# Kernel tuning notes

Hardware: AMD Instinct MI355X
Metric: run time of the kernel (lower is better)

The kernel has to match this reference:

```python
import jax, jax.numpy as jnp
import numpy as np

T, B, L, CTX, H = 512, 512, 16, 64, 128
STATE_DIM, SHOT, PID, DATA = 32, 12, 35, 23


def setup_inputs() -> dict:
    key = jax.random.key(0)
    ks = jax.random.split(key, 64)
    k = iter(ks)
    def rn(shape, s=0.1):
        return (jax.random.normal(next(k), shape) * s).astype(jnp.float32)
    xs = jax.random.normal(next(k), (T, B, DATA), jnp.float32)
    xs = xs.at[:, :, 12].set(jax.random.randint(next(k), (T, B), 0, SHOT).astype(jnp.float32))
    xs = xs.at[:, :, 17].set(jax.random.randint(next(k), (T, B), 0, PID).astype(jnp.float32))
    xs = xs.at[:, :, 20].set(jax.random.randint(next(k), (T, B), 0, SHOT).astype(jnp.float32))
    return dict(
        total_xs=jnp.zeros((1,), jnp.float32),
        xs=xs,
        ts=jnp.linspace(0.0, 2.0, T).astype(jnp.float32),
        noise_std=jnp.asarray(0.1, jnp.float32),
        z0_noise=jax.random.normal(next(k), (B, L), jnp.float32),
        bm_noise=jax.random.normal(next(k), (T - 1, B, L), jnp.float32),
        shot_emb=rn((SHOT, 8)), player_emb=rn((PID, 8)),
        gru_wih=rn((3 * H, STATE_DIM)), gru_whh=rn((3 * H, H)),
        gru_bih=rn((3 * H,)), gru_bhh=rn((3 * H,)),
        enc_w=rn((CTX, H)), enc_b=rn((CTX,)),
        qz0_w=rn((2 * L, CTX)), qz0_b=rn((2 * L,)),
        f_w1=rn((H, L + CTX)), f_b1=rn((H,)), f_w2=rn((H, H)), f_b2=rn((H,)),
        f_w3=rn((L, H)), f_b3=rn((L,)),
        h_w1=rn((H, L)), h_b1=rn((H,)), h_w2=rn((H, H)), h_b2=rn((H,)),
        h_w3=rn((L, H)), h_b3=rn((L,)),
        g_w1=rn((L, H)), g_b1=rn((L, H)), g_w2=rn((L, H)), g_b2=rn((L,)),
        proj_w=rn((STATE_DIM, L)), proj_b=rn((STATE_DIM,)),
        pz0_mean=jnp.zeros((1, L), jnp.float32), pz0_logstd=jnp.zeros((1, L), jnp.float32),
        act_w=rn((128, L)), act_b=rn((128,)),
        act_land_w=rn((2, 128)), act_shot_w=rn((SHOT, 128)), act_move_w=rn((2, 128)),
    )


def _forward(xs, noise_std, shot_emb, player_emb, gru_wih, gru_whh, gru_bih, gru_bhh,
             enc_w, enc_b, qz0_w, qz0_b,
             f_w1, f_b1, f_w2, f_b2, f_w3, f_b3,
             h_w1, h_b1, h_w2, h_b2, h_w3, h_b3,
             g_w1, g_b1, g_w2, g_b2,
             proj_w, proj_b, pz0_mean, pz0_logstd,
             act_w, act_b, act_land_w, act_shot_w, act_move_w,
             ts, z0_noise, bm_noise):
    # --- SDE_embed_and_transform: replace shot/player id cols with embeddings ---
    state = xs[:, :, :18]
    shot_ids = state[:, :, 12].astype(jnp.int32)
    pid_ids = state[:, :, 17].astype(jnp.int32)
    state_t = jnp.concatenate([state[:, :, :12], shot_emb[shot_ids],
                               state[:, :, 13:17], player_emb[pid_ids]], axis=-1)  # (T,B,32)
    xs_t = jnp.concatenate([state_t, xs[:, :, 18:]], axis=-1)  # (T,B,37)
    # --- Encoder: GRU over time-reversed states, linear head, flip back ---
    def gru_step(h, xt):
        gi = xt @ gru_wih.T + gru_bih
        gh = h @ gru_whh.T + gru_bhh
        ir, iz, inn = jnp.split(gi, 3, axis=-1)
        hr, hz, hn = jnp.split(gh, 3, axis=-1)
        r = jax.nn.sigmoid(ir + hr)
        zg = jax.nn.sigmoid(iz + hz)
        n = jnp.tanh(inn + r * hn)
        hnew = (1.0 - zg) * n + zg * h
        return hnew, hnew
    h0 = jnp.zeros((xs.shape[1], gru_whh.shape[1]), xs.dtype)
    _, hs = jax.lax.scan(gru_step, h0, state_t[::-1])
    ctx = (hs @ enc_w.T + enc_b)[::-1]  # (T,B,CTX)
    # --- posterior z0 ---
    qm, qls = jnp.split(ctx[0] @ qz0_w.T + qz0_b, 2, axis=1)
    z0 = qm + jnp.exp(qls) * z0_noise
    # --- Euler-Maruyama with logqp; searchsorted(right) -> ctx[min(i+1,T-1)] = ctx[i+1] ---
    dts = ts[1:] - ts[:-1]  # (T-1,)
    dW = jnp.sqrt(dts)[:, None, None] * bm_noise
    ctx_steps = ctx[1:]
    def mlp3(x, w1, b1, w2, b2, w3, b3):
        h1 = jax.nn.softplus(x @ w1.T + b1)
        h2 = jax.nn.softplus(h1 @ w2.T + b2)
        return h2 @ w3.T + b3
    def g_diag(y):  # (B,L): per-latent-dim scalar nets, batched over L
        hg = jax.nn.softplus(y[:, :, None] * g_w1[None] + g_b1[None])  # (B,L,H)
        return jax.nn.sigmoid(jnp.einsum('blh,lh->bl', hg, g_w2) + g_b2)
    def sde_step(z, inp):
        c, dw, dt = inp
        f_val = mlp3(jnp.concatenate([z, c], axis=1), f_w1, f_b1, f_w2, f_b2, f_w3, f_b3)
        h_val = mlp3(z, h_w1, h_b1, h_w2, h_b2, h_w3, h_b3)
        g_val = g_diag(z)
        u = (f_val - h_val) / g_val
        logr = 0.5 * jnp.sum(u * u, axis=1) * dt
        z_new = z + f_val * dt + g_val * dw
        return z_new, (z_new, logr)
    _, (z_tail, log_ratio) = jax.lax.scan(sde_step, z0, (ctx_steps, dW, dts))
    zs = jnp.concatenate([z0[None], z_tail], axis=0)  # (T,B,L)
    _xs = zs @ proj_w.T + proj_b  # (T,B,32)
    # --- action model losses ---
    a = jax.nn.relu(zs @ act_w.T + act_b)
    land = (a @ act_land_w.T).reshape(-1, 2)
    shot_logits = (a @ act_shot_w.T).reshape(-1, act_shot_w.shape[0])
    move = (a @ act_move_w.T).reshape(-1, 2)
    true_actions = xs_t[:, :, -5:]
    true_land = true_actions[:, :, :2].reshape(-1, 2)
    true_move = true_actions[:, :, 3:].reshape(-1, 2)
    true_shot = true_actions[:, :, 2].astype(jnp.int32).reshape(-1)
    land_loss = jnp.mean((land - true_land) ** 2)
    move_loss = jnp.mean((move - true_move) ** 2)
    logp = jax.nn.log_softmax(shot_logits, axis=-1)
    picked = jnp.take_along_axis(logp, true_shot[:, None], axis=1)[:, 0]
    mask = (true_shot != 0).astype(logp.dtype)  # CrossEntropy ignore_index=0
    shot_loss = -jnp.sum(picked * mask) / jnp.maximum(jnp.sum(mask), 1.0)
    # --- reconstruction log-likelihood ---
    xs_state = xs_t[:, :, :STATE_DIM]
    LOG2PI = 1.8378770664093453
    log_pxs = jnp.mean(jnp.sum(
        -0.5 * ((xs_state - _xs) / noise_std) ** 2 - jnp.log(noise_std) - 0.5 * LOG2PI,
        axis=(0, 2)))
    # --- KL(q(z0) || p(z0)) ---
    var_q = jnp.exp(2.0 * qls)
    var_p = jnp.exp(2.0 * pz0_logstd)
    kl = pz0_logstd - qls + (var_q + (qm - pz0_mean) ** 2) / (2.0 * var_p) - 0.5
    logqp0 = jnp.mean(jnp.sum(kl, axis=1))
    logqp_path = jnp.mean(jnp.sum(log_ratio, axis=0))
    return log_pxs, logqp0 + logqp_path + land_loss + shot_loss + move_loss


def reference(total_xs, xs, ts, noise_std, z0_noise, bm_noise, shot_emb, player_emb,
              gru_wih, gru_whh, gru_bih, gru_bhh, enc_w, enc_b, qz0_w, qz0_b,
              f_w1, f_b1, f_w2, f_b2, f_w3, f_b3, h_w1, h_b1, h_w2, h_b2, h_w3, h_b3,
              g_w1, g_b1, g_w2, g_b2, proj_w, proj_b, pz0_mean, pz0_logstd,
              act_w, act_b, act_land_w, act_shot_w, act_move_w):
    return _forward(xs, noise_std, shot_emb, player_emb, gru_wih, gru_whh, gru_bih, gru_bhh,
                    enc_w, enc_b, qz0_w, qz0_b,
                    f_w1, f_b1, f_w2, f_b2, f_w3, f_b3,
                    h_w1, h_b1, h_w2, h_b2, h_w3, h_b3,
                    g_w1, g_b1, g_w2, g_b2,
                    proj_w, proj_b, pz0_mean, pz0_logstd,
                    act_w, act_b, act_land_w, act_shot_w, act_move_w,
                    ts, z0_noise, bm_noise)
```

## Files before the change

kernel.cpp:

```cpp
#include <hip/hip_runtime.h>
#include <cstdint>

typedef _Float16 f16;
typedef _Float16 f16x2 __attribute__((ext_vector_type(2)));

#define T_STEPS 512
#define B_SZ 512
#define LOG2PI 1.8378770664093453f

__device__ __forceinline__ uint32_t packh2(float a, float b) {
  f16x2 v; v[0] = (f16)a; v[1] = (f16)b;
  return __builtin_bit_cast(uint32_t, v);
}

__device__ __forceinline__ float fdot2(uint32_t a, uint32_t b, float c) {
#if defined(__AMDGCN__) && __has_builtin(__builtin_amdgcn_fdot2)
  return __builtin_amdgcn_fdot2(__builtin_bit_cast(f16x2, a),
                                __builtin_bit_cast(f16x2, b), c, false);
#else
  f16x2 x = __builtin_bit_cast(f16x2, a), y = __builtin_bit_cast(f16x2, b);
  return c + (float)x[0] * (float)y[0] + (float)x[1] * (float)y[1];
#endif
}

#define DOT4(acc, w0, w1, w2, w3, v)                                     \
  do {                                                                   \
    acc = fdot2((w0), (v).x, acc); acc = fdot2((w1), (v).y, acc);        \
    acc = fdot2((w2), (v).z, acc); acc = fdot2((w3), (v).w, acc);        \
  } while (0)

__device__ __forceinline__ float sigmoidf_(float x) {
  return 1.0f / (1.0f + __expf(-x));
}
__device__ __forceinline__ float tanhf_(float x) {
  float ax = fabsf(x);
  float t = __expf(-2.0f * ax);
  float r = (1.0f - t) / (1.0f + t);
  return copysignf(r, x);
}
__device__ __forceinline__ float softplusf_(float x) {
  return fmaxf(x, 0.0f) + __logf(1.0f + __expf(-fabsf(x)));
}

__global__ __launch_bounds__(256) void k_embed(
    const float* __restrict__ xs, const float* __restrict__ shot_emb,
    const float* __restrict__ player_emb, f16* __restrict__ state_t,
    float* __restrict__ accums) {
  if (blockIdx.x == 0 && threadIdx.x < 16) accums[threadIdx.x] = 0.0f;
  size_t idx = (size_t)blockIdx.x * 256 + threadIdx.x;
  const float* xp = xs + idx * 23;
  f16* op = state_t + idx * 32;
  int sid = (int)xp[12];
  int pid = (int)xp[17];
#pragma unroll
  for (int i = 0; i < 12; ++i) op[i] = (f16)xp[i];
  const float* se = shot_emb + sid * 8;
#pragma unroll
  for (int i = 0; i < 8; ++i) op[12 + i] = (f16)se[i];
#pragma unroll
  for (int i = 0; i < 4; ++i) op[20 + i] = (f16)xp[13 + i];
  const float* pe = player_emb + pid * 8;
#pragma unroll
  for (int i = 0; i < 8; ++i) op[24 + i] = (f16)pe[i];
}

__global__ __launch_bounds__(512) void k_gru(
    const f16* __restrict__ state_t, const float* __restrict__ wih,
    const float* __restrict__ whh, const float* __restrict__ bih,
    const float* __restrict__ bhh, const float* __restrict__ enc_w,
    const float* __restrict__ enc_b, const float* __restrict__ qz0_w,
    const float* __restrict__ qz0_b, const float* __restrict__ z0_noise,
    const float* __restrict__ pz0_mean, const float* __restrict__ pz0_logstd,
    f16* __restrict__ ctx, float* __restrict__ z0_out,
    float* __restrict__ accums) {
  __shared__ uint32_t s_x[2][16];
  __shared__ uint32_t s_h[2][64];
  __shared__ float s_gates[2 * 128 * 4];
  __shared__ float s_encp[2 * 64 * 2];
  __shared__ float s_ctx0[2][64];
  __shared__ float s_q[2][32];

  const int tid = threadIdx.x;
  const int bbase = blockIdx.x * 2;
  const uint32_t* stu = (const uint32_t*)state_t;

  uint32_t wA[64];
  uint32_t wB[16];
  float bias0 = 0.f, bias1 = 0.f, encbr = 0.f;

  if (tid < 256) {
    int g = tid >> 7, du = tid & 127;
    const float* whr = whh + (size_t)(g * 128 + du) * 128;
#pragma unroll
    for (int i = 0; i < 64; ++i) wA[i] = packh2(whr[2 * i], whr[2 * i + 1]);
    const float* wxr = wih + (size_t)(g * 128 + du) * 32;
#pragma unroll
    for (int i = 0; i < 16; ++i) wB[i] = packh2(wxr[2 * i], wxr[2 * i + 1]);
    bias0 = bih[g * 128 + du] + bhh[g * 128 + du];
  } else if (tid < 384) {
    int du = tid - 256;
    const float* whr = whh + (size_t)(256 + du) * 128;
#pragma unroll
    for (int i = 0; i < 64; ++i) wA[i] = packh2(whr[2 * i], whr[2 * i + 1]);
    const float* wxr = wih + (size_t)(256 + du) * 32;
#pragma unroll
    for (int i = 0; i < 16; ++i) wB[i] = packh2(wxr[2 * i], wxr[2 * i + 1]);
    bias0 = bih[256 + du];
    bias1 = bhh[256 + du];
  } else {
    int e = tid - 384, c = e & 63, ks = e >> 6;
    const float* wer = enc_w + (size_t)c * 128 + ks * 64;
#pragma unroll
    for (int i = 0; i < 32; ++i) wA[i] = packh2(wer[2 * i], wer[2 * i + 1]);
    encbr = enc_b[c];
  }

  if (tid < 128) s_h[tid >> 6][tid & 63] = 0u;
  if (tid < 32) {
    int b = tid >> 4, i = tid & 15;
    s_x[b][i] = stu[((size_t)(T_STEPS - 1) * B_SZ + bbase + b) * 16 + i];
  }
  float h_old = 0.0f;
  __syncthreads();

  for (int t = T_STEPS - 1; t >= 0; --t) {
    uint4 xpref = make_uint4(0, 0, 0, 0);
    if (tid < 256) {
      int g = tid >> 7, du = tid & 127;
#pragma unroll
      for (int b = 0; b < 2; ++b) {
        float a = bias0;
        const uint4* xq = (const uint4*)&s_x[b][0];
#pragma unroll
        for (int j = 0; j < 4; ++j) {
          uint4 v = xq[j];
          DOT4(a, wB[4 * j], wB[4 * j + 1], wB[4 * j + 2], wB[4 * j + 3], v);
        }
        const uint4* hq = (const uint4*)&s_h[b][0];
#pragma unroll
        for (int j = 0; j < 16; ++j) {
          uint4 v = hq[j];
          DOT4(a, wA[4 * j], wA[4 * j + 1], wA[4 * j + 2], wA[4 * j + 3], v);
        }
        s_gates[(b * 128 + du) * 4 + g] = a;
      }
    } else if (tid < 384) {
      int du = tid - 256;
#pragma unroll
      for (int b = 0; b < 2; ++b) {
        float aI = bias0, aH = bias1;
        const uint4* xq = (const uint4*)&s_x[b][0];
#pragma unroll
        for (int j = 0; j < 4; ++j) {
          uint4 v = xq[j];
          DOT4(aI, wB[4 * j], wB[4 * j + 1], wB[4 * j + 2], wB[4 * j + 3], v);
        }
        const uint4* hq = (const uint4*)&s_h[b][0];
#pragma unroll
        for (int j = 0; j < 16; ++j) {
          uint4 v = hq[j];
          DOT4(aH, wA[4 * j], wA[4 * j + 1], wA[4 * j + 2], wA[4 * j + 3], v);
        }
        s_gates[(b * 128 + du) * 4 + 2] = aI;
        s_gates[(b * 128 + du) * 4 + 3] = aH;
      }
    } else {
      int e = tid - 384, ks = e >> 6, cc = e & 63;
      (void)cc;
      if (t < T_STEPS - 1) {
#pragma unroll
        for (int b = 0; b < 2; ++b) {
          float a = 0.f;
          const uint4* hq = (const uint4*)&s_h[b][ks * 32];
#pragma unroll
          for (int j = 0; j < 8; ++j) {
            uint4 v = hq[j];
            DOT4(a, wA[4 * j], wA[4 * j + 1], wA[4 * j + 2], wA[4 * j + 3], v);
          }
          s_encp[(b * 64 + cc) * 2 + ks] = a;
        }
      }
      if (e < 8 && t > 0) {
        int b = e & 1, q = e >> 1;
        xpref = *(const uint4*)(stu +
                                ((size_t)(t - 1) * B_SZ + bbase + b) * 16 + q * 4);
      }
    }
    __syncthreads();
    if (tid < 256) {
      int b = tid >> 7, du = tid & 127;
      const float4 gt = *(const float4*)&s_gates[(b * 128 + du) * 4];
      float r = sigmoidf_(gt.x), zg = sigmoidf_(gt.y);
      float n = tanhf_(gt.z + r * gt.w);
      float hnew = (1.0f - zg) * n + zg * h_old;
      h_old = hnew;
      ((f16*)&s_h[b][0])[du] = (f16)hnew;
    } else if (tid >= 384) {
      int e = tid - 384, cc = e & 63, b = e >> 6;
      if (t < T_STEPS - 1) {
        float2 p = *(const float2*)&s_encp[(b * 64 + cc) * 2];
        ctx[((size_t)(t + 1) * B_SZ + bbase + b) * 64 + cc] =
            (f16)(p.x + p.y + encbr);
      }
      if (e < 8 && t > 0) {
        int b2 = e & 1, q = e >> 1;
        *(uint4*)&s_x[b2][q * 4] = xpref;
      }
    }
    __syncthreads();
  }

  if (tid >= 384) {
    int e = tid - 384, ks = e >> 6, cc = e & 63;
#pragma unroll
    for (int b = 0; b < 2; ++b) {
      float a = 0.f;
      const uint4* hq = (const uint4*)&s_h[b][ks * 32];
#pragma unroll
      for (int j = 0; j < 8; ++j) {
        uint4 v = hq[j];
        DOT4(a, wA[4 * j], wA[4 * j + 1], wA[4 * j + 2], wA[4 * j + 3], v);
      }
      s_encp[(b * 64 + cc) * 2 + ks] = a;
    }
  }
  __syncthreads();
  if (tid >= 384) {
    int e = tid - 384, cc = e & 63, b = e >> 6;
    float2 p = *(const float2*)&s_encp[(b * 64 + cc) * 2];
    float val = p.x + p.y + encbr;
    ctx[((size_t)bbase + b) * 64 + cc] = (f16)val;
    s_ctx0[b][cc] = val;
  }
  __syncthreads();
  if (tid < 64) {
    int b = tid >> 5, o = tid & 31;
    float acc = qz0_b[o];
#pragma unroll 8
    for (int k = 0; k < 64; ++k) acc += qz0_w[o * 64 + k] * s_ctx0[b][k];
    s_q[b][o] = acc;
  }
  __syncthreads();
  if (tid < 32) {
    int b = tid >> 4, l = tid & 15;
    int bg = bbase + b;
    float qm = s_q[b][l], qls = s_q[b][16 + l];
    float z0v = qm + __expf(qls) * z0_noise[bg * 16 + l];
    z0_out[bg * 16 + l] = z0v;
    float pm = pz0_mean[l], pls = pz0_logstd[l];
    float var_q = __expf(2.0f * qls);
    float var_p = __expf(2.0f * pls);
    float dm = qm - pm;
    float kl = pls - qls + (var_q + dm * dm) / (2.0f * var_p) - 0.5f;
    atomicAdd(&accums[5], kl);
  }
}

__global__ __launch_bounds__(512) void k_sde(
    const f16* __restrict__ ctx, const float* __restrict__ z0_in,
    const float* __restrict__ ts, const float* __restrict__ bm_noise,
    const float* __restrict__ fw1, const float* __restrict__ fb1,
    const float* __restrict__ fw2, const float* __restrict__ fb2,
    const float* __restrict__ fw3, const float* __restrict__ fb3,
    const float* __restrict__ hw1, const float* __restrict__ hb1,
    const float* __restrict__ hw2, const float* __restrict__ hb2,
    const float* __restrict__ hw3, const float* __restrict__ hb3,
    const float* __restrict__ gw1, const float* __restrict__ gb1,
    const float* __restrict__ gw2, const float* __restrict__ gb2,
    f16* __restrict__ zs, float* __restrict__ accums) {
  __shared__ uint32_t s_x2[2][40];
  __shared__ float s_zf[2][16];
  __shared__ uint32_t s_h1[2][2][64];
  __shared__ uint32_t s_h2[2][2][64];
  __shared__ float s_gp[256];
  __shared__ float s_gv[32];
  __shared__ float s_p2[2 * 2 * 128 * 2];
  __shared__ float s_p3[2 * 2 * 16 * 8];
  __shared__ float s_dts[512];

  const int tid = threadIdx.x;
  const int bbase = blockIdx.x * 2;

  uint32_t uw[48];
  uint32_t wP2[32];
  uint32_t wP3[8];
  float bias1r = 0.f, bias2r = 0.f, gb2r = 0.f, fb3r = 0.f, hb3r = 0.f;

  if (tid < 256) {
    int l = tid & 15, k8 = (tid >> 4) & 7;
#pragma unroll
    for (int i = 0; i < 16; ++i) {
      int h = k8 * 16 + i;
      uw[i] = __builtin_bit_cast(uint32_t, gw1[l * 128 + h]);
      uw[16 + i] = __builtin_bit_cast(uint32_t, gb1[l * 128 + h]);
      uw[32 + i] = __builtin_bit_cast(uint32_t, gw2[l * 128 + h]);
    }
  } else if (tid < 384) {
    int u = tid - 256;
    const float* w = fw1 + (size_t)u * 80;
#pragma unroll
    for (int i = 0; i < 40; ++i) uw[i] = packh2(w[2 * i], w[2 * i + 1]);
    bias1r = fb1[u];
  } else {
    int u = tid - 384;
    const float* w = hw1 + (size_t)u * 16;
#pragma unroll
    for (int i = 0; i < 8; ++i) uw[i] = packh2(w[2 * i], w[2 * i + 1]);
    bias1r = hb1[u];
  }
  {
    int u = tid & 127, ks = (tid >> 7) & 1, mlp = tid >> 8;
    const float* w = (mlp ? hw2 : fw2) + (size_t)u * 128 + ks * 64;
#pragma unroll
    for (int i = 0; i < 32; ++i) wP2[i] = packh2(w[2 * i], w[2 * i + 1]);
    bias2r = (mlp ? hb2 : fb2)[u];
  }
  if (tid < 128 || (tid >= 256 && tid < 384)) {
    int o = tid & 15, k8 = (tid >> 4) & 7;
    const float* w = ((tid >= 256) ? hw3 : fw3) + (size_t)o * 128 + k8 * 16;
#pragma unroll
    for (int i = 0; i < 8; ++i) wP3[i] = packh2(w[2 * i], w[2 * i + 1]);
  }
  if (tid >= 128 && tid < 160) gb2r = gb2[tid & 15];
  if (tid < 32) {
    fb3r = fb3[tid & 15];
    hb3r = hb3[tid & 15];
  }

  if (tid < 511) s_dts[tid] = ts[tid + 1] - ts[tid];
  float bmc = 0.f;
  uint4 cpref = make_uint4(0, 0, 0, 0);
  if (tid < 32) {
    int b = tid >> 4, l = tid & 15, bg = bbase + b;
    float z = z0_in[bg * 16 + l];
    s_zf[b][l] = z;
    ((f16*)&s_x2[b][0])[l] = (f16)z;
    zs[(size_t)bg * 16 + l] = (f16)z;
    bmc = bm_noise[((size_t)0 * B_SZ + bg) * 16 + l];
  }
  if (tid >= 32 && tid < 48) {
    int i = tid - 32, b = i & 1, q = i >> 1;
    const uint32_t* cu = (const uint32_t*)ctx;
    uint4 v = *(const uint4*)(cu + ((size_t)1 * B_SZ + bbase + b) * 32 + q * 4);
    *(uint4*)&s_x2[b][8 + q * 4] = v;
  }
  float path_acc = 0.0f;
  __syncthreads();

  for (int t = 0; t < T_STEPS - 1; ++t) {
    float bmn = 0.f;
    if (tid < 32 && t < T_STEPS - 2) {
      int b = tid >> 4, l = tid & 15, bg = bbase + b;
      bmn = bm_noise[((size_t)(t + 1) * B_SZ + bg) * 16 + l];
    }
    if (tid >= 32 && tid < 48 && t <= T_STEPS - 3) {
      int i = tid - 32, b = i & 1, q = i >> 1;
      const uint32_t* cu = (const uint32_t*)ctx;
      cpref = *(const uint4*)(cu +
                              ((size_t)(t + 2) * B_SZ + bbase + b) * 32 + q * 4);
    }
    if (tid < 256) {
      int b = tid >> 7, l = tid & 15, k8 = (tid >> 4) & 7;
      float y = s_zf[b][l];
      float acc = 0.f;
#pragma unroll
      for (int i = 0; i < 16; ++i) {
        float pre = fmaf(y, __builtin_bit_cast(float, uw[i]),
                         __builtin_bit_cast(float, uw[16 + i]));
        acc = fmaf(softplusf_(pre), __builtin_bit_cast(float, uw[32 + i]), acc);
      }
      s_gp[(b * 16 + l) * 8 + k8] = acc;
    } else if (tid < 384) {
      int u = tid - 256;
#pragma unroll
      for (int b = 0; b < 2; ++b) {
        float a = bias1r;
        const uint4* xq = (const uint4*)&s_x2[b][0];
#pragma unroll
        for (int j = 0; j < 10; ++j) {
          uint4 v = xq[j];
          DOT4(a, uw[4 * j], uw[4 * j + 1], uw[4 * j + 2], uw[4 * j + 3], v);
        }
        ((f16*)&s_h1[0][b][0])[u] = (f16)softplusf_(a);
      }
    } else {
      int u = tid - 384;
#pragma unroll
      for (int b = 0; b < 2; ++b) {
        float a = bias1r;
        const uint4* xq = (const uint4*)&s_x2[b][0];
#pragma unroll
        for (int j = 0; j < 2; ++j) {
          uint4 v = xq[j];
          DOT4(a, uw[4 * j], uw[4 * j + 1], uw[4 * j + 2], uw[4 * j + 3], v);
        }
        ((f16*)&s_h1[1][b][0])[u] = (f16)softplusf_(a);
      }
    }
    __syncthreads();
    {
      int u = tid & 127, ks = (tid >> 7) & 1, mlp = tid >> 8;
#pragma unroll
      for (int b = 0; b < 2; ++b) {
        float a = 0.f;
        const uint4* hq = (const uint4*)&s_h1[mlp][b][ks * 32];
#pragma unroll
        for (int j = 0; j < 8; ++j) {
          uint4 v = hq[j];
          DOT4(a, wP2[4 * j], wP2[4 * j + 1], wP2[4 * j + 2], wP2[4 * j + 3], v);
        }
        s_p2[((mlp * 2 + b) * 128 + u) * 2 + ks] = a;
      }
    }
    __syncthreads();
    {
      int u = tid & 127, b = (tid >> 7) & 1, mlp = tid >> 8;
      float2 p = *(const float2*)&s_p2[((mlp * 2 + b) * 128 + u) * 2];
      ((f16*)&s_h2[mlp][b][0])[u] = (f16)softplusf_(p.x + p.y + bias2r);
    }
    __syncthreads();
    if (tid < 128 || (tid >= 256 && tid < 384)) {
      int o = tid & 15, k8 = (tid >> 4) & 7, mlp = tid >> 8;
#pragma unroll
      for (int b = 0; b < 2; ++b) {
        float a = 0.f;
        const uint4* hq = (const uint4*)&s_h2[mlp][b][k8 * 8];
#pragma unroll
        for (int j = 0; j < 2; ++j) {
          uint4 v = hq[j];
          DOT4(a, wP3[4 * j], wP3[4 * j + 1], wP3[4 * j + 2], wP3[4 * j + 3], v);
        }
        s_p3[((mlp * 2 + b) * 16 + o) * 8 + k8] = a;
      }
    } else if (tid >= 128 && tid < 160) {
      int i = tid - 128, b = i >> 4, l = i & 15;
      const float4* gp = (const float4*)&s_gp[(b * 16 + l) * 8];
      float4 g0 = gp[0], g1 = gp[1];
      float sum = g0.x + g0.y + g0.z + g0.w + g1.x + g1.y + g1.z + g1.w + gb2r;
      s_gv[b * 16 + l] = sigmoidf_(sum);
    }
    __syncthreads();
    if (tid < 32) {
      int b = tid >> 4, l = tid & 15, bg = bbase + b;
      const float4* fp = (const float4*)&s_p3[((0 * 2 + b) * 16 + l) * 8];
      const float4* hp = (const float4*)&s_p3[((2 + b) * 16 + l) * 8];
      float4 f0 = fp[0], f1v = fp[1], h0 = hp[0], h1v = hp[1];
      float fv = fb3r + f0.x + f0.y + f0.z + f0.w + f1v.x + f1v.y + f1v.z + f1v.w;
      float hv = hb3r + h0.x + h0.y + h0.z + h0.w + h1v.x + h1v.y + h1v.z + h1v.w;
      float gv = s_gv[b * 16 + l];
      float dt = s_dts[t];
      float u = (fv - hv) / gv;
      float lsum = u * u;
      lsum += __shfl_xor(lsum, 1);
      lsum += __shfl_xor(lsum, 2);
      lsum += __shfl_xor(lsum, 4);
      lsum += __shfl_xor(lsum, 8);
      if (l == 0) path_acc += 0.5f * lsum * dt;
      float dw = sqrtf(dt) * bmc;
      float zn = s_zf[b][l] + fv * dt + gv * dw;
      s_zf[b][l] = zn;
      ((f16*)&s_x2[b][0])[l] = (f16)zn;
      zs[((size_t)(t + 1) * B_SZ + bg) * 16 + l] = (f16)zn;
      bmc = bmn;
    } else if (tid >= 32 && tid < 48 && t <= T_STEPS - 3) {
      int i = tid - 32, b = i & 1, q = i >> 1;
      *(uint4*)&s_x2[b][8 + q * 4] = cpref;
    }
    __syncthreads();
  }
  if (tid < 32 && (tid & 15) == 0) atomicAdd(&accums[6], path_acc);
}

__global__ __launch_bounds__(256) void k_dec(
    const f16* __restrict__ zs, const f16* __restrict__ state_t,
    const float* __restrict__ xs, const float* __restrict__ proj_w,
    const float* __restrict__ proj_b, const float* __restrict__ act_w,
    const float* __restrict__ act_b, const float* __restrict__ land_w,
    const float* __restrict__ shot_w, const float* __restrict__ move_w,
    float* __restrict__ accums) {
  __shared__ uint32_t s_proj[8 * 32];
  __shared__ uint32_t s_act[8 * 128];
  __shared__ uint32_t s_head[128 * 8];
  __shared__ float s_pb[32], s_ab[128];
  __shared__ float s_red[4 * 5];

  const int tid = threadIdx.x;
  for (int id = tid; id < 8 * 32; id += 256) {
    int kp = id & 7, n = id >> 3;
    s_proj[kp * 32 + n] = packh2(proj_w[n * 16 + 2 * kp], proj_w[n * 16 + 2 * kp + 1]);
  }
  for (int id = tid; id < 8 * 128; id += 256) {
    int kp = id & 7, n = id >> 3;
    s_act[kp * 128 + n] = packh2(act_w[n * 16 + 2 * kp], act_w[n * 16 + 2 * kp + 1]);
  }
  for (int id = tid; id < 128 * 8; id += 256) {
    int j = id >> 3, p = id & 7;
    int h0 = 2 * p, h1 = 2 * p + 1;
    float w0 = (h0 < 2) ? land_w[h0 * 128 + j]
                        : (h0 < 14 ? shot_w[(h0 - 2) * 128 + j]
                                   : move_w[(h0 - 14) * 128 + j]);
    float w1 = (h1 < 2) ? land_w[h1 * 128 + j]
                        : (h1 < 14 ? shot_w[(h1 - 2) * 128 + j]
                                   : move_w[(h1 - 14) * 128 + j]);
    s_head[j * 8 + p] = packh2(w0, w1);
  }
  if (tid < 32) s_pb[tid] = proj_b[tid];
  if (tid < 128) s_ab[tid] = act_b[tid];
  __syncthreads();

  size_t idx = (size_t)blockIdx.x * 256 + tid;
  uint32_t z2[8];
  const uint32_t* zp = (const uint32_t*)(zs + idx * 16);
#pragma unroll
  for (int i = 0; i < 8; ++i) z2[i] = zp[i];
  uint32_t stv[16];
  const uint32_t* stp = (const uint32_t*)(state_t + idx * 32);
#pragma unroll
  for (int i = 0; i < 16; ++i) stv[i] = stp[i];

  float sqsum = 0.0f;
#pragma unroll 4
  for (int i = 0; i < 32; ++i) {
    float acc = s_pb[i];
#pragma unroll
    for (int kp = 0; kp < 8; ++kp) acc = fdot2(s_proj[kp * 32 + i], z2[kp], acc);
    f16x2 sv = __builtin_bit_cast(f16x2, stv[i >> 1]);
    float d = (float)sv[i & 1] - acc;
    sqsum += d * d;
  }

  float hd[16];
#pragma unroll
  for (int i = 0; i < 16; ++i) hd[i] = 0.0f;
#pragma unroll 2
  for (int j = 0; j < 128; ++j) {
    float a = s_ab[j];
#pragma unroll
    for (int kp = 0; kp < 8; ++kp) a = fdot2(s_act[kp * 128 + j], z2[kp], a);
    a = fmaxf(a, 0.0f);
#pragma unroll
    for (int p = 0; p < 8; ++p) {
      f16x2 w = __builtin_bit_cast(f16x2, s_head[j * 8 + p]);
      hd[2 * p] += (float)w[0] * a;
      hd[2 * p + 1] += (float)w[1] * a;
    }
  }
  const float* xp = xs + idx * 23;
  float dl0 = hd[0] - xp[18], dl1 = hd[1] - xp[19];
  float land = dl0 * dl0 + dl1 * dl1;
  float dm0 = hd[14] - xp[21], dm1 = hd[15] - xp[22];
  float move = dm0 * dm0 + dm1 * dm1;
  int sid = (int)xp[20];
  float m = hd[2];
#pragma unroll
  for (int s = 1; s < 12; ++s) m = fmaxf(m, hd[2 + s]);
  float sume = 0.0f;
#pragma unroll
  for (int s = 0; s < 12; ++s) sume += __expf(hd[2 + s] - m);
  float lse = m + __logf(sume);
  float pl = 0.0f;
#pragma unroll
  for (int s = 0; s < 12; ++s)
    if (s == sid) pl = hd[2 + s];
  float picked = 0.0f, cnt = 0.0f;
  if (sid != 0) {
    picked = pl - lse;
    cnt = 1.0f;
  }
  float vals[5] = {sqsum, land, move, picked, cnt};
#pragma unroll
  for (int v = 0; v < 5; ++v) {
    float x = vals[v];
    for (int off = 1; off < 64; off <<= 1) x += __shfl_xor(x, off);
    vals[v] = x;
  }
  int lane = tid & 63, wv = tid >> 6;
  if (lane == 0) {
#pragma unroll
    for (int v = 0; v < 5; ++v) s_red[wv * 5 + v] = vals[v];
  }
  __syncthreads();
  if (tid == 0) {
#pragma unroll
    for (int v = 0; v < 5; ++v) {
      float s = s_red[v] + s_red[5 + v] + s_red[10 + v] + s_red[15 + v];
      atomicAdd(&accums[v], s);
    }
  }
}

__global__ void k_fin(const float* __restrict__ accums,
                      const float* __restrict__ noise_std,
                      float* __restrict__ out) {
  if (threadIdx.x == 0 && blockIdx.x == 0) {
    float sd = noise_std[0];
    float log_pxs = -0.5f * accums[0] / (sd * sd * (float)B_SZ) -
                    (float)T_STEPS * 32.0f * (logf(sd) + 0.5f * LOG2PI);
    float land = accums[1] / (float)(T_STEPS * B_SZ * 2);
    float move = accums[2] / (float)(T_STEPS * B_SZ * 2);
    float shot = -accums[3] / fmaxf(accums[4], 1.0f);
    float out1 = accums[5] / (float)B_SZ + accums[6] / (float)B_SZ + land + shot + move;
    out[0] = log_pxs;
    out[1] = out1;
  }
}

extern "C" void kernel_launch(void* const* d_in, const int* in_sizes, int n_in,
                              void* d_out, int out_size, void* d_ws,
                              size_t ws_size, hipStream_t stream) {
  const float* xs = (const float*)d_in[1];
  const float* ts = (const float*)d_in[2];
  const float* noise_std = (const float*)d_in[3];
  const float* z0_noise = (const float*)d_in[4];
  const float* bm_noise = (const float*)d_in[5];
  const float* shot_emb = (const float*)d_in[6];
  const float* player_emb = (const float*)d_in[7];
  const float* gru_wih = (const float*)d_in[8];
  const float* gru_whh = (const float*)d_in[9];
  const float* gru_bih = (const float*)d_in[10];
  const float* gru_bhh = (const float*)d_in[11];
  const float* enc_w = (const float*)d_in[12];
  const float* enc_b = (const float*)d_in[13];
  const float* qz0_w = (const float*)d_in[14];
  const float* qz0_b = (const float*)d_in[15];
  const float* f_w1 = (const float*)d_in[16];
  const float* f_b1 = (const float*)d_in[17];
  const float* f_w2 = (const float*)d_in[18];
  const float* f_b2 = (const float*)d_in[19];
  const float* f_w3 = (const float*)d_in[20];
  const float* f_b3 = (const float*)d_in[21];
  const float* h_w1 = (const float*)d_in[22];
  const float* h_b1 = (const float*)d_in[23];
  const float* h_w2 = (const float*)d_in[24];
  const float* h_b2 = (const float*)d_in[25];
  const float* h_w3 = (const float*)d_in[26];
  const float* h_b3 = (const float*)d_in[27];
  const float* g_w1 = (const float*)d_in[28];
  const float* g_b1 = (const float*)d_in[29];
  const float* g_w2 = (const float*)d_in[30];
  const float* g_b2 = (const float*)d_in[31];
  const float* proj_w = (const float*)d_in[32];
  const float* proj_b = (const float*)d_in[33];
  const float* pz0_mean = (const float*)d_in[34];
  const float* pz0_logstd = (const float*)d_in[35];
  const float* act_w = (const float*)d_in[36];
  const float* act_b = (const float*)d_in[37];
  const float* act_land_w = (const float*)d_in[38];
  const float* act_shot_w = (const float*)d_in[39];
  const float* act_move_w = (const float*)d_in[40];

  char* ws = (char*)d_ws;
  float* accums = (float*)ws;
  f16* state_t = (f16*)(ws + 256);
  f16* ctx = (f16*)(ws + 256 + 16777216);
  float* z0b = (float*)(ws + 256 + 16777216 + 33554432);
  f16* zs = (f16*)(ws + 256 + 16777216 + 33554432 + 32768);

  k_embed<<<1024, 256, 0, stream>>>(xs, shot_emb, player_emb, state_t, accums);
  k_gru<<<256, 512, 0, stream>>>(state_t, gru_wih, gru_whh, gru_bih, gru_bhh,
                                 enc_w, enc_b, qz0_w, qz0_b, z0_noise, pz0_mean,
                                 pz0_logstd, ctx, z0b, accums);
  k_sde<<<256, 512, 0, stream>>>(ctx, z0b, ts, bm_noise, f_w1, f_b1, f_w2, f_b2,
                                 f_w3, f_b3, h_w1, h_b1, h_w2, h_b2, h_w3, h_b3,
                                 g_w1, g_b1, g_w2, g_b2, zs, accums);
  k_dec<<<1024, 256, 0, stream>>>(zs, state_t, xs, proj_w, proj_b, act_w, act_b,
                                  act_land_w, act_shot_w, act_move_w, accums);
  k_fin<<<1, 64, 0, stream>>>(accums, noise_std, (float*)d_out);
}
```

Before: 1.999 ms.

## Assign one batch element per block in GRU and SDE, two tokens per thread in decoder

The GRU and SDE recurrent kernels change from two batch elements per block to one, doubling the grid to 512 blocks and shrinking block sizes (448 and 256 threads) with occupancy launch bounds. Each thread now does a full-length dot product with two split accumulators, which removes the partial-sum scratch buffers and gate interleaving. The decoder processes two tokens per thread with vectorized shared-memory weight layouts, reusing each weight load across both tokens. The aim is more parallelism across CUs and shorter serial dependency chains per recurrence step. The cost is more registers per thread and duplicated weight loading across twice as many blocks.

```diff
diff --git a/kernel.cpp b/kernel.cpp
--- a/kernel.cpp
+++ b/kernel.cpp
@@ -64,7 +64,7 @@
   for (int i = 0; i < 8; ++i) op[24 + i] = (f16)pe[i];
 }
 
-__global__ __launch_bounds__(512) void k_gru(
+__global__ __launch_bounds__(448, 4) void k_gru(
     const f16* __restrict__ state_t, const float* __restrict__ wih,
     const float* __restrict__ whh, const float* __restrict__ bih,
     const float* __restrict__ bhh, const float* __restrict__ enc_w,
@@ -73,181 +73,121 @@
     const float* __restrict__ pz0_mean, const float* __restrict__ pz0_logstd,
     f16* __restrict__ ctx, float* __restrict__ z0_out,
     float* __restrict__ accums) {
-  __shared__ uint32_t s_x[2][16];
-  __shared__ uint32_t s_h[2][64];
-  __shared__ float s_gates[2 * 128 * 4];
-  __shared__ float s_encp[2 * 64 * 2];
-  __shared__ float s_ctx0[2][64];
-  __shared__ float s_q[2][32];
+  __shared__ __align__(16) uint32_t s_x[16];
+  __shared__ __align__(16) uint32_t s_h[64];
+  __shared__ float s_gi[384], s_gh[384];
+  __shared__ float s_ctx0[64];
+  __shared__ float s_q[32];
 
   const int tid = threadIdx.x;
-  const int bbase = blockIdx.x * 2;
+  const int bg = blockIdx.x;
   const uint32_t* stu = (const uint32_t*)state_t;
 
   uint32_t wA[64];
   uint32_t wB[16];
-  float bias0 = 0.f, bias1 = 0.f, encbr = 0.f;
-
-  if (tid < 256) {
-    int g = tid >> 7, du = tid & 127;
-    const float* whr = whh + (size_t)(g * 128 + du) * 128;
+  float bi = 0.f, bh = 0.f, encbr = 0.f;
+
+  if (tid < 384) {
+    const float* whr = whh + (size_t)tid * 128;
 #pragma unroll
     for (int i = 0; i < 64; ++i) wA[i] = packh2(whr[2 * i], whr[2 * i + 1]);
-    const float* wxr = wih + (size_t)(g * 128 + du) * 32;
+    const float* wxr = wih + (size_t)tid * 32;
 #pragma unroll
     for (int i = 0; i < 16; ++i) wB[i] = packh2(wxr[2 * i], wxr[2 * i + 1]);
-    bias0 = bih[g * 128 + du] + bhh[g * 128 + du];
-  } else if (tid < 384) {
-    int du = tid - 256;
-    const float* whr = whh + (size_t)(256 + du) * 128;
-#pragma unroll
-    for (int i = 0; i < 64; ++i) wA[i] = packh2(whr[2 * i], whr[2 * i + 1]);
-    const float* wxr = wih + (size_t)(256 + du) * 32;
-#pragma unroll
-    for (int i = 0; i < 16; ++i) wB[i] = packh2(wxr[2 * i], wxr[2 * i + 1]);
-    bias0 = bih[256 + du];
-    bias1 = bhh[256 + du];
+    bi = bih[tid];
+    bh = bhh[tid];
   } else {
-    int e = tid - 384, c = e & 63, ks = e >> 6;
-    const float* wer = enc_w + (size_t)c * 128 + ks * 64;
-#pragma unroll
-    for (int i = 0; i < 32; ++i) wA[i] = packh2(wer[2 * i], wer[2 * i + 1]);
-    encbr = enc_b[c];
-  }
-
-  if (tid < 128) s_h[tid >> 6][tid & 63] = 0u;
-  if (tid < 32) {
-    int b = tid >> 4, i = tid & 15;
-    s_x[b][i] = stu[((size_t)(T_STEPS - 1) * B_SZ + bbase + b) * 16 + i];
-  }
+    int cc = tid - 384;
+    const float* wer = enc_w + (size_t)cc * 128;
+#pragma unroll
+    for (int i = 0; i < 64; ++i) wA[i] = packh2(wer[2 * i], wer[2 * i + 1]);
+    encbr = enc_b[cc];
+  }
+
+  if (tid < 64) s_h[tid] = 0u;
+  if (tid < 4)
+    *(uint4*)&s_x[tid * 4] =
+        *(const uint4*)(stu + ((size_t)(T_STEPS - 1) * B_SZ + bg) * 16 + tid * 4);
   float h_old = 0.0f;
   __syncthreads();
 
   for (int t = T_STEPS - 1; t >= 0; --t) {
     uint4 xpref = make_uint4(0, 0, 0, 0);
-    if (tid < 256) {
-      int g = tid >> 7, du = tid & 127;
-#pragma unroll
-      for (int b = 0; b < 2; ++b) {
-        float a = bias0;
-        const uint4* xq = (const uint4*)&s_x[b][0];
-#pragma unroll
-        for (int j = 0; j < 4; ++j) {
-          uint4 v = xq[j];
-          DOT4(a, wB[4 * j], wB[4 * j + 1], wB[4 * j + 2], wB[4 * j + 3], v);
-        }
-        const uint4* hq = (const uint4*)&s_h[b][0];
-#pragma unroll
-        for (int j = 0; j < 16; ++j) {
-          uint4 v = hq[j];
-          DOT4(a, wA[4 * j], wA[4 * j + 1], wA[4 * j + 2], wA[4 * j + 3], v);
-        }
-        s_gates[(b * 128 + du) * 4 + g] = a;
+    if (tid >= 128 && tid < 132 && t > 0)
+      xpref = *(const uint4*)(stu + ((size_t)(t - 1) * B_SZ + bg) * 16 +
+                              (tid - 128) * 4);
+    if (tid < 384) {
+      float ax0 = bi, ax1 = 0.f;
+      const uint4* xq = (const uint4*)s_x;
+#pragma unroll
+      for (int j = 0; j < 4; ++j) {
+        uint4 v = xq[j];
+        if (j & 1) { DOT4(ax1, wB[4 * j], wB[4 * j + 1], wB[4 * j + 2], wB[4 * j + 3], v); }
+        else       { DOT4(ax0, wB[4 * j], wB[4 * j + 1], wB[4 * j + 2], wB[4 * j + 3], v); }
       }
-    } else if (tid < 384) {
-      int du = tid - 256;
-#pragma unroll
-      for (int b = 0; b < 2; ++b) {
-        float aI = bias0, aH = bias1;
-        const uint4* xq = (const uint4*)&s_x[b][0];
-#pragma unroll
-        for (int j = 0; j < 4; ++j) {
-          uint4 v = xq[j];
-          DOT4(aI, wB[4 * j], wB[4 * j + 1], wB[4 * j + 2], wB[4 * j + 3], v);
-        }
-        const uint4* hq = (const uint4*)&s_h[b][0];
-#pragma unroll
-        for (int j = 0; j < 16; ++j) {
-          uint4 v = hq[j];
-          DOT4(aH, wA[4 * j], wA[4 * j + 1], wA[4 * j + 2], wA[4 * j + 3], v);
-        }
-        s_gates[(b * 128 + du) * 4 + 2] = aI;
-        s_gates[(b * 128 + du) * 4 + 3] = aH;
+      float ah0 = bh, ah1 = 0.f;
+      const uint4* hq = (const uint4*)s_h;
+#pragma unroll
+      for (int j = 0; j < 16; ++j) {
+        uint4 v = hq[j];
+        if (j & 1) { DOT4(ah1, wA[4 * j], wA[4 * j + 1], wA[4 * j + 2], wA[4 * j + 3], v); }
+        else       { DOT4(ah0, wA[4 * j], wA[4 * j + 1], wA[4 * j + 2], wA[4 * j + 3], v); }
       }
-    } else {
-      int e = tid - 384, ks = e >> 6, cc = e & 63;
-      (void)cc;
-      if (t < T_STEPS - 1) {
-#pragma unroll
-        for (int b = 0; b < 2; ++b) {
-          float a = 0.f;
-          const uint4* hq = (const uint4*)&s_h[b][ks * 32];
-#pragma unroll
-          for (int j = 0; j < 8; ++j) {
-            uint4 v = hq[j];
-            DOT4(a, wA[4 * j], wA[4 * j + 1], wA[4 * j + 2], wA[4 * j + 3], v);
-          }
-          s_encp[(b * 64 + cc) * 2 + ks] = a;
-        }
+      s_gi[tid] = ax0 + ax1;
+      s_gh[tid] = ah0 + ah1;
+    } else if (t < T_STEPS - 1) {
+      int cc = tid - 384;
+      float a0 = encbr, a1 = 0.f;
+      const uint4* hq = (const uint4*)s_h;
+#pragma unroll
+      for (int j = 0; j < 16; ++j) {
+        uint4 v = hq[j];
+        if (j & 1) { DOT4(a1, wA[4 * j], wA[4 * j + 1], wA[4 * j + 2], wA[4 * j + 3], v); }
+        else       { DOT4(a0, wA[4 * j], wA[4 * j + 1], wA[4 * j + 2], wA[4 * j + 3], v); }
       }
-      if (e < 8 && t > 0) {
-        int b = e & 1, q = e >> 1;
-        xpref = *(const uint4*)(stu +
-                                ((size_t)(t - 1) * B_SZ + bbase + b) * 16 + q * 4);
-      }
+      ctx[((size_t)(t + 1) * B_SZ + bg) * 64 + cc] = (f16)(a0 + a1);
     }
     __syncthreads();
-    if (tid < 256) {
-      int b = tid >> 7, du = tid & 127;
-      const float4 gt = *(const float4*)&s_gates[(b * 128 + du) * 4];
-      float r = sigmoidf_(gt.x), zg = sigmoidf_(gt.y);
-      float n = tanhf_(gt.z + r * gt.w);
+    if (tid < 128) {
+      float r = sigmoidf_(s_gi[tid] + s_gh[tid]);
+      float zg = sigmoidf_(s_gi[128 + tid] + s_gh[128 + tid]);
+      float n = tanhf_(s_gi[256 + tid] + r * s_gh[256 + tid]);
       float hnew = (1.0f - zg) * n + zg * h_old;
       h_old = hnew;
-      ((f16*)&s_h[b][0])[du] = (f16)hnew;
-    } else if (tid >= 384) {
-      int e = tid - 384, cc = e & 63, b = e >> 6;
-      if (t < T_STEPS - 1) {
-        float2 p = *(const float2*)&s_encp[(b * 64 + cc) * 2];
-        ctx[((size_t)(t + 1) * B_SZ + bbase + b) * 64 + cc] =
-            (f16)(p.x + p.y + encbr);
-      }
-      if (e < 8 && t > 0) {
-        int b2 = e & 1, q = e >> 1;
-        *(uint4*)&s_x[b2][q * 4] = xpref;
-      }
+      ((f16*)s_h)[tid] = (f16)hnew;
+    } else if (tid >= 128 && tid < 132 && t > 0) {
+      *(uint4*)&s_x[(tid - 128) * 4] = xpref;
     }
     __syncthreads();
   }
 
   if (tid >= 384) {
-    int e = tid - 384, ks = e >> 6, cc = e & 63;
-#pragma unroll
-    for (int b = 0; b < 2; ++b) {
-      float a = 0.f;
-      const uint4* hq = (const uint4*)&s_h[b][ks * 32];
-#pragma unroll
-      for (int j = 0; j < 8; ++j) {
-        uint4 v = hq[j];
-        DOT4(a, wA[4 * j], wA[4 * j + 1], wA[4 * j + 2], wA[4 * j + 3], v);
-      }
-      s_encp[(b * 64 + cc) * 2 + ks] = a;
-    }
-  }
-  __syncthreads();
-  if (tid >= 384) {
-    int e = tid - 384, cc = e & 63, b = e >> 6;
-    float2 p = *(const float2*)&s_encp[(b * 64 + cc) * 2];
-    float val = p.x + p.y + encbr;
-    ctx[((size_t)bbase + b) * 64 + cc] = (f16)val;
-    s_ctx0[b][cc] = val;
-  }
-  __syncthreads();
-  if (tid < 64) {
-    int b = tid >> 5, o = tid & 31;
-    float acc = qz0_b[o];
-#pragma unroll 8
-    for (int k = 0; k < 64; ++k) acc += qz0_w[o * 64 + k] * s_ctx0[b][k];
-    s_q[b][o] = acc;
+    int cc = tid - 384;
+    float a0 = encbr, a1 = 0.f;
+    const uint4* hq = (const uint4*)s_h;
+#pragma unroll
+    for (int j = 0; j < 16; ++j) {
+      uint4 v = hq[j];
+      if (j & 1) { DOT4(a1, wA[4 * j], wA[4 * j + 1], wA[4 * j + 2], wA[4 * j + 3], v); }
+      else       { DOT4(a0, wA[4 * j], wA[4 * j + 1], wA[4 * j + 2], wA[4 * j + 3], v); }
+    }
+    float val = a0 + a1;
+    ctx[(size_t)bg * 64 + cc] = (f16)val;
+    s_ctx0[cc] = val;
   }
   __syncthreads();
   if (tid < 32) {
-    int b = tid >> 4, l = tid & 15;
-    int bg = bbase + b;
-    float qm = s_q[b][l], qls = s_q[b][16 + l];
-    float z0v = qm + __expf(qls) * z0_noise[bg * 16 + l];
-    z0_out[bg * 16 + l] = z0v;
-    float pm = pz0_mean[l], pls = pz0_logstd[l];
+    float acc = qz0_b[tid];
+#pragma unroll 8
+    for (int k = 0; k < 64; ++k) acc += qz0_w[tid * 64 + k] * s_ctx0[k];
+    s_q[tid] = acc;
+  }
+  __syncthreads();
+  if (tid < 16) {
+    float qm = s_q[tid], qls = s_q[16 + tid];
+    float z0v = qm + __expf(qls) * z0_noise[bg * 16 + tid];
+    z0_out[bg * 16 + tid] = z0v;
+    float pm = pz0_mean[tid], pls = pz0_logstd[tid];
     float var_q = __expf(2.0f * qls);
     float var_p = __expf(2.0f * pls);
     float dm = qm - pm;
@@ -256,7 +196,7 @@
   }
 }
 
-__global__ __launch_bounds__(512) void k_sde(
+__global__ __launch_bounds__(256, 2) void k_sde(
     const f16* __restrict__ ctx, const float* __restrict__ z0_in,
     const float* __restrict__ ts, const float* __restrict__ bm_noise,
     const float* __restrict__ fw1, const float* __restrict__ fb1,
@@ -268,186 +208,153 @@
     const float* __restrict__ gw1, const float* __restrict__ gb1,
     const float* __restrict__ gw2, const float* __restrict__ gb2,
     f16* __restrict__ zs, float* __restrict__ accums) {
-  __shared__ uint32_t s_x2[2][40];
-  __shared__ float s_zf[2][16];
-  __shared__ uint32_t s_h1[2][2][64];
-  __shared__ uint32_t s_h2[2][2][64];
-  __shared__ float s_gp[256];
-  __shared__ float s_gv[32];
-  __shared__ float s_p2[2 * 2 * 128 * 2];
-  __shared__ float s_p3[2 * 2 * 16 * 8];
-  __shared__ float s_dts[512];
+  __shared__ __align__(16) uint32_t s_x2[40];
+  __shared__ __align__(16) uint32_t s_h1f[64];
+  __shared__ __align__(16) uint32_t s_h1h[64];
+  __shared__ __align__(16) uint32_t s_h2[2][64];
+  __shared__ float s_zf[16];
+  __shared__ __align__(16) float s_gp[128];
+  __shared__ __align__(16) float s_p3[256];
+  __shared__ float s_dts[T_STEPS];
 
   const int tid = threadIdx.x;
-  const int bbase = blockIdx.x * 2;
-
-  uint32_t uw[48];
-  uint32_t wP2[32];
+  const int bg = blockIdx.x;
+
+  uint32_t uw[56];
+  uint32_t wP2[64];
   uint32_t wP3[8];
   float bias1r = 0.f, bias2r = 0.f, gb2r = 0.f, fb3r = 0.f, hb3r = 0.f;
 
-  if (tid < 256) {
-    int l = tid & 15, k8 = (tid >> 4) & 7;
+  if (tid < 128) {
+    const float* w = fw1 + (size_t)tid * 80;
+#pragma unroll
+    for (int i = 0; i < 40; ++i) uw[i] = packh2(w[2 * i], w[2 * i + 1]);
+    bias1r = fb1[tid];
+  } else {
+    int u = tid - 128;
+    const float* w = hw1 + (size_t)u * 16;
+#pragma unroll
+    for (int i = 0; i < 8; ++i) uw[i] = packh2(w[2 * i], w[2 * i + 1]);
+    bias1r = hb1[u];
+    int l = u & 15, k8 = u >> 4;
 #pragma unroll
     for (int i = 0; i < 16; ++i) {
       int h = k8 * 16 + i;
-      uw[i] = __builtin_bit_cast(uint32_t, gw1[l * 128 + h]);
-      uw[16 + i] = __builtin_bit_cast(uint32_t, gb1[l * 128 + h]);
-      uw[32 + i] = __builtin_bit_cast(uint32_t, gw2[l * 128 + h]);
-    }
-  } else if (tid < 384) {
-    int u = tid - 256;
-    const float* w = fw1 + (size_t)u * 80;
-#pragma unroll
-    for (int i = 0; i < 40; ++i) uw[i] = packh2(w[2 * i], w[2 * i + 1]);
-    bias1r = fb1[u];
-  } else {
-    int u = tid - 384;
-    const float* w = hw1 + (size_t)u * 16;
-#pragma unroll
-    for (int i = 0; i < 8; ++i) uw[i] = packh2(w[2 * i], w[2 * i + 1]);
-    bias1r = hb1[u];
+      uw[8 + i] = __builtin_bit_cast(uint32_t, gw1[l * 128 + h]);
+      uw[24 + i] = __builtin_bit_cast(uint32_t, gb1[l * 128 + h]);
+      uw[40 + i] = __builtin_bit_cast(uint32_t, gw2[l * 128 + h]);
+    }
   }
   {
-    int u = tid & 127, ks = (tid >> 7) & 1, mlp = tid >> 8;
-    const float* w = (mlp ? hw2 : fw2) + (size_t)u * 128 + ks * 64;
-#pragma unroll
-    for (int i = 0; i < 32; ++i) wP2[i] = packh2(w[2 * i], w[2 * i + 1]);
+    int mlp = tid >> 7, u = tid & 127;
+    const float* w = (mlp ? hw2 : fw2) + (size_t)u * 128;
+#pragma unroll
+    for (int i = 0; i < 64; ++i) wP2[i] = packh2(w[2 * i], w[2 * i + 1]);
     bias2r = (mlp ? hb2 : fb2)[u];
   }
-  if (tid < 128 || (tid >= 256 && tid < 384)) {
-    int o = tid & 15, k8 = (tid >> 4) & 7;
-    const float* w = ((tid >= 256) ? hw3 : fw3) + (size_t)o * 128 + k8 * 16;
+  {
+    int mlp = tid >> 7, o = tid & 15, k8 = (tid >> 4) & 7;
+    const float* w = (mlp ? hw3 : fw3) + (size_t)o * 128 + k8 * 16;
 #pragma unroll
     for (int i = 0; i < 8; ++i) wP3[i] = packh2(w[2 * i], w[2 * i + 1]);
   }
-  if (tid >= 128 && tid < 160) gb2r = gb2[tid & 15];
-  if (tid < 32) {
-    fb3r = fb3[tid & 15];
-    hb3r = hb3[tid & 15];
-  }
-
-  if (tid < 511) s_dts[tid] = ts[tid + 1] - ts[tid];
-  float bmc = 0.f;
-  uint4 cpref = make_uint4(0, 0, 0, 0);
-  if (tid < 32) {
-    int b = tid >> 4, l = tid & 15, bg = bbase + b;
-    float z = z0_in[bg * 16 + l];
-    s_zf[b][l] = z;
-    ((f16*)&s_x2[b][0])[l] = (f16)z;
-    zs[(size_t)bg * 16 + l] = (f16)z;
-    bmc = bm_noise[((size_t)0 * B_SZ + bg) * 16 + l];
-  }
-  if (tid >= 32 && tid < 48) {
-    int i = tid - 32, b = i & 1, q = i >> 1;
-    const uint32_t* cu = (const uint32_t*)ctx;
-    uint4 v = *(const uint4*)(cu + ((size_t)1 * B_SZ + bbase + b) * 32 + q * 4);
-    *(uint4*)&s_x2[b][8 + q * 4] = v;
+  if (tid < 16) {
+    fb3r = fb3[tid];
+    hb3r = hb3[tid];
+    gb2r = gb2[tid];
+  }
+  for (int i = tid; i < T_STEPS - 1; i += 256) s_dts[i] = ts[i + 1] - ts[i];
+
+  if (tid < 16) {
+    float z = z0_in[bg * 16 + tid];
+    s_zf[tid] = z;
+    ((f16*)s_x2)[tid] = (f16)z;
+    zs[(size_t)bg * 16 + tid] = (f16)z;
+  }
+  if (tid >= 16 && tid < 24) {
+    int q = tid - 16;
+    *(uint4*)&s_x2[8 + q * 4] =
+        *(const uint4*)((const uint32_t*)ctx + ((size_t)1 * B_SZ + bg) * 32 + q * 4);
   }
   float path_acc = 0.0f;
   __syncthreads();
 
   for (int t = 0; t < T_STEPS - 1; ++t) {
-    float bmn = 0.f;
-    if (tid < 32 && t < T_STEPS - 2) {
-      int b = tid >> 4, l = tid & 15, bg = bbase + b;
-      bmn = bm_noise[((size_t)(t + 1) * B_SZ + bg) * 16 + l];
-    }
-    if (tid >= 32 && tid < 48 && t <= T_STEPS - 3) {
-      int i = tid - 32, b = i & 1, q = i >> 1;
-      const uint32_t* cu = (const uint32_t*)ctx;
-      cpref = *(const uint4*)(cu +
-                              ((size_t)(t + 2) * B_SZ + bbase + b) * 32 + q * 4);
-    }
-    if (tid < 256) {
-      int b = tid >> 7, l = tid & 15, k8 = (tid >> 4) & 7;
-      float y = s_zf[b][l];
+    float bm_cur = 0.f;
+    uint4 cpref = make_uint4(0, 0, 0, 0);
+    if (tid < 16) bm_cur = bm_noise[((size_t)t * B_SZ + bg) * 16 + tid];
+    if (tid >= 16 && tid < 24 && t <= T_STEPS - 3) {
+      int q = tid - 16;
+      cpref = *(const uint4*)((const uint32_t*)ctx +
+                              ((size_t)(t + 2) * B_SZ + bg) * 32 + q * 4);
+    }
+    if (tid < 128) {
+      float a0 = bias1r, a1 = 0.f;
+      const uint4* xq = (const uint4*)s_x2;
+#pragma unroll
+      for (int j = 0; j < 10; ++j) {
+        uint4 v = xq[j];
+        if (j & 1) { DOT4(a1, uw[4 * j], uw[4 * j + 1], uw[4 * j + 2], uw[4 * j + 3], v); }
+        else       { DOT4(a0, uw[4 * j], uw[4 * j + 1], uw[4 * j + 2], uw[4 * j + 3], v); }
+      }
+      ((f16*)s_h1f)[tid] = (f16)softplusf_(a0 + a1);
+    } else {
+      int u = tid - 128;
+      const uint4* zq = (const uint4*)s_x2;
+      float a0 = bias1r, a1 = 0.f;
+      uint4 v0 = zq[0], v1 = zq[1];
+      DOT4(a0, uw[0], uw[1], uw[2], uw[3], v0);
+      DOT4(a1, uw[4], uw[5], uw[6], uw[7], v1);
+      ((f16*)s_h1h)[u] = (f16)softplusf_(a0 + a1);
+      int l = u & 15, k8 = u >> 4;
+      float y = s_zf[l];
       float acc = 0.f;
 #pragma unroll
       for (int i = 0; i < 16; ++i) {
-        float pre = fmaf(y, __builtin_bit_cast(float, uw[i]),
-                         __builtin_bit_cast(float, uw[16 + i]));
-        acc = fmaf(softplusf_(pre), __builtin_bit_cast(float, uw[32 + i]), acc);
+        float pre = fmaf(y, __builtin_bit_cast(float, uw[8 + i]),
+                         __builtin_bit_cast(float, uw[24 + i]));
+        acc = fmaf(softplusf_(pre), __builtin_bit_cast(float, uw[40 + i]), acc);
       }
-      s_gp[(b * 16 + l) * 8 + k8] = acc;
-    } else if (tid < 384) {
-      int u = tid - 256;
-#pragma unroll
-      for (int b = 0; b < 2; ++b) {
-        float a = bias1r;
-        const uint4* xq = (const uint4*)&s_x2[b][0];
-#pragma unroll
-        for (int j = 0; j < 10; ++j) {
-          uint4 v = xq[j];
-          DOT4(a, uw[4 * j], uw[4 * j + 1], uw[4 * j + 2], uw[4 * j + 3], v);
-        }
-        ((f16*)&s_h1[0][b][0])[u] = (f16)softplusf_(a);
-      }
-    } else {
-      int u = tid - 384;
-#pragma unroll
-      for (int b = 0; b < 2; ++b) {
-        float a = bias1r;
-        const uint4* xq = (const uint4*)&s_x2[b][0];
-#pragma unroll
-        for (int j = 0; j < 2; ++j) {
-          uint4 v = xq[j];
-          DOT4(a, uw[4 * j], uw[4 * j + 1], uw[4 * j + 2], uw[4 * j + 3], v);
-        }
-        ((f16*)&s_h1[1][b][0])[u] = (f16)softplusf_(a);
-      }
+      s_gp[l * 8 + k8] = acc;
     }
     __syncthreads();
     {
-      int u = tid & 127, ks = (tid >> 7) & 1, mlp = tid >> 8;
-#pragma unroll
-      for (int b = 0; b < 2; ++b) {
-        float a = 0.f;
-        const uint4* hq = (const uint4*)&s_h1[mlp][b][ks * 32];
-#pragma unroll
-        for (int j = 0; j < 8; ++j) {
-          uint4 v = hq[j];
-          DOT4(a, wP2[4 * j], wP2[4 * j + 1], wP2[4 * j + 2], wP2[4 * j + 3], v);
-        }
-        s_p2[((mlp * 2 + b) * 128 + u) * 2 + ks] = a;
+      const uint4* hq = (const uint4*)((tid >> 7) ? s_h1h : s_h1f);
+      float a0 = bias2r, a1 = 0.f, a2 = 0.f, a3 = 0.f;
+#pragma unroll
+      for (int j = 0; j < 16; j += 4) {
+        uint4 v0 = hq[j], v1 = hq[j + 1], v2 = hq[j + 2], v3 = hq[j + 3];
+        DOT4(a0, wP2[4 * j], wP2[4 * j + 1], wP2[4 * j + 2], wP2[4 * j + 3], v0);
+        DOT4(a1, wP2[4 * j + 4], wP2[4 * j + 5], wP2[4 * j + 6], wP2[4 * j + 7], v1);
+        DOT4(a2, wP2[4 * j + 8], wP2[4 * j + 9], wP2[4 * j + 10], wP2[4 * j + 11], v2);
+        DOT4(a3, wP2[4 * j + 12], wP2[4 * j + 13], wP2[4 * j + 14], wP2[4 * j + 15], v3);
       }
+      ((f16*)s_h2[tid >> 7])[tid & 127] = (f16)softplusf_((a0 + a1) + (a2 + a3));
     }
     __syncthreads();
     {
-      int u = tid & 127, b = (tid >> 7) & 1, mlp = tid >> 8;
-      float2 p = *(const float2*)&s_p2[((mlp * 2 + b) * 128 + u) * 2];
-      ((f16*)&s_h2[mlp][b][0])[u] = (f16)softplusf_(p.x + p.y + bias2r);
+      int mlp = tid >> 7, o = tid & 15, k8 = (tid >> 4) & 7;
+      const uint4* hq = (const uint4*)&s_h2[mlp][k8 * 8];
+      uint4 v0 = hq[0], v1 = hq[1];
+      float a0 = 0.f, a1 = 0.f;
+      DOT4(a0, wP3[0], wP3[1], wP3[2], wP3[3], v0);
+      DOT4(a1, wP3[4], wP3[5], wP3[6], wP3[7], v1);
+      s_p3[(mlp * 16 + o) * 8 + k8] = a0 + a1;
     }
     __syncthreads();
-    if (tid < 128 || (tid >= 256 && tid < 384)) {
-      int o = tid & 15, k8 = (tid >> 4) & 7, mlp = tid >> 8;
-#pragma unroll
-      for (int b = 0; b < 2; ++b) {
-        float a = 0.f;
-        const uint4* hq = (const uint4*)&s_h2[mlp][b][k8 * 8];
-#pragma unroll
-        for (int j = 0; j < 2; ++j) {
-          uint4 v = hq[j];
-          DOT4(a, wP3[4 * j], wP3[4 * j + 1], wP3[4 * j + 2], wP3[4 * j + 3], v);
-        }
-        s_p3[((mlp * 2 + b) * 16 + o) * 8 + k8] = a;
-      }
-    } else if (tid >= 128 && tid < 160) {
-      int i = tid - 128, b = i >> 4, l = i & 15;
-      const float4* gp = (const float4*)&s_gp[(b * 16 + l) * 8];
+    if (tid < 16) {
+      int l = tid;
+      const float4* fp = (const float4*)&s_p3[l * 8];
+      const float4* hp = (const float4*)&s_p3[(16 + l) * 8];
+      const float4* gp = (const float4*)&s_gp[l * 8];
+      float4 f0 = fp[0], f1v = fp[1], h0 = hp[0], h1v = hp[1];
       float4 g0 = gp[0], g1 = gp[1];
-      float sum = g0.x + g0.y + g0.z + g0.w + g1.x + g1.y + g1.z + g1.w + gb2r;
-      s_gv[b * 16 + l] = sigmoidf_(sum);
-    }
-    __syncthreads();
-    if (tid < 32) {
-      int b = tid >> 4, l = tid & 15, bg = bbase + b;
-      const float4* fp = (const float4*)&s_p3[((0 * 2 + b) * 16 + l) * 8];
-      const float4* hp = (const float4*)&s_p3[((2 + b) * 16 + l) * 8];
-      float4 f0 = fp[0], f1v = fp[1], h0 = hp[0], h1v = hp[1];
-      float fv = fb3r + f0.x + f0.y + f0.z + f0.w + f1v.x + f1v.y + f1v.z + f1v.w;
-      float hv = hb3r + h0.x + h0.y + h0.z + h0.w + h1v.x + h1v.y + h1v.z + h1v.w;
-      float gv = s_gv[b * 16 + l];
+      float fv = fb3r + ((f0.x + f0.y) + (f0.z + f0.w)) +
+                 ((f1v.x + f1v.y) + (f1v.z + f1v.w));
+      float hv = hb3r + ((h0.x + h0.y) + (h0.z + h0.w)) +
+                 ((h1v.x + h1v.y) + (h1v.z + h1v.w));
+      float gv = sigmoidf_(gb2r + ((g0.x + g0.y) + (g0.z + g0.w)) +
+                           ((g1.x + g1.y) + (g1.z + g1.w)));
       float dt = s_dts[t];
       float u = (fv - hv) / gv;
       float lsum = u * u;
@@ -456,19 +363,17 @@
       lsum += __shfl_xor(lsum, 4);
       lsum += __shfl_xor(lsum, 8);
       if (l == 0) path_acc += 0.5f * lsum * dt;
-      float dw = sqrtf(dt) * bmc;
-      float zn = s_zf[b][l] + fv * dt + gv * dw;
-      s_zf[b][l] = zn;
-      ((f16*)&s_x2[b][0])[l] = (f16)zn;
+      float zn = s_zf[l] + fv * dt + gv * (sqrtf(dt) * bm_cur);
+      s_zf[l] = zn;
+      ((f16*)s_x2)[l] = (f16)zn;
       zs[((size_t)(t + 1) * B_SZ + bg) * 16 + l] = (f16)zn;
-      bmc = bmn;
-    } else if (tid >= 32 && tid < 48 && t <= T_STEPS - 3) {
-      int i = tid - 32, b = i & 1, q = i >> 1;
-      *(uint4*)&s_x2[b][8 + q * 4] = cpref;
+    } else if (tid >= 16 && tid < 24 && t <= T_STEPS - 3) {
+      int q = tid - 16;
+      *(uint4*)&s_x2[8 + q * 4] = cpref;
     }
     __syncthreads();
   }
-  if (tid < 32 && (tid & 15) == 0) atomicAdd(&accums[6], path_acc);
+  if (tid == 0) atomicAdd(&accums[6], path_acc);
 }
 
 __global__ __launch_bounds__(256) void k_dec(
@@ -478,22 +383,22 @@
     const float* __restrict__ act_b, const float* __restrict__ land_w,
     const float* __restrict__ shot_w, const float* __restrict__ move_w,
     float* __restrict__ accums) {
-  __shared__ uint32_t s_proj[8 * 32];
-  __shared__ uint32_t s_act[8 * 128];
-  __shared__ uint32_t s_head[128 * 8];
+  __shared__ __align__(16) uint32_t s_proj[32 * 8];
+  __shared__ __align__(16) uint32_t s_act[128 * 8];
+  __shared__ __align__(16) uint32_t s_head[128 * 8];
   __shared__ float s_pb[32], s_ab[128];
   __shared__ float s_red[4 * 5];
 
   const int tid = threadIdx.x;
-  for (int id = tid; id < 8 * 32; id += 256) {
-    int kp = id & 7, n = id >> 3;
-    s_proj[kp * 32 + n] = packh2(proj_w[n * 16 + 2 * kp], proj_w[n * 16 + 2 * kp + 1]);
-  }
-  for (int id = tid; id < 8 * 128; id += 256) {
-    int kp = id & 7, n = id >> 3;
-    s_act[kp * 128 + n] = packh2(act_w[n * 16 + 2 * kp], act_w[n * 16 + 2 * kp + 1]);
-  }
-  for (int id = tid; id < 128 * 8; id += 256) {
+  if (tid < 256) {
+    int i = tid >> 3, kp = tid & 7;
+    s_proj[tid] = packh2(proj_w[i * 16 + 2 * kp], proj_w[i * 16 + 2 * kp + 1]);
+  }
+  for (int id = tid; id < 1024; id += 256) {
+    int j = id >> 3, kp = id & 7;
+    s_act[id] = packh2(act_w[j * 16 + 2 * kp], act_w[j * 16 + 2 * kp + 1]);
+  }
+  for (int id = tid; id < 1024; id += 256) {
     int j = id >> 3, p = id & 7;
     int h0 = 2 * p, h1 = 2 * p + 1;
     float w0 = (h0 < 2) ? land_w[h0 * 128 + j]
@@ -508,66 +413,102 @@
   if (tid < 128) s_ab[tid] = act_b[tid];
   __syncthreads();
 
-  size_t idx = (size_t)blockIdx.x * 256 + tid;
-  uint32_t z2[8];
-  const uint32_t* zp = (const uint32_t*)(zs + idx * 16);
-#pragma unroll
-  for (int i = 0; i < 8; ++i) z2[i] = zp[i];
-  uint32_t stv[16];
-  const uint32_t* stp = (const uint32_t*)(state_t + idx * 32);
-#pragma unroll
-  for (int i = 0; i < 16; ++i) stv[i] = stp[i];
-
-  float sqsum = 0.0f;
+  size_t idx0 = (size_t)blockIdx.x * 512 + tid;
+  size_t idx1 = idx0 + 256;
+  uint32_t zA[8], zB[8];
+  {
+    const uint4* za = (const uint4*)(zs + idx0 * 16);
+    const uint4* zb = (const uint4*)(zs + idx1 * 16);
+    uint4 a0 = za[0], a1 = za[1], b0 = zb[0], b1 = zb[1];
+    zA[0] = a0.x; zA[1] = a0.y; zA[2] = a0.z; zA[3] = a0.w;
+    zA[4] = a1.x; zA[5] = a1.y; zA[6] = a1.z; zA[7] = a1.w;
+    zB[0] = b0.x; zB[1] = b0.y; zB[2] = b0.z; zB[3] = b0.w;
+    zB[4] = b1.x; zB[5] = b1.y; zB[6] = b1.z; zB[7] = b1.w;
+  }
+  uint32_t stA[16], stB[16];
+  {
+    const uint4* sa = (const uint4*)(state_t + idx0 * 32);
+    const uint4* sb = (const uint4*)(state_t + idx1 * 32);
+#pragma unroll
+    for (int q = 0; q < 4; ++q) {
+      uint4 va = sa[q], vb = sb[q];
+      stA[4 * q] = va.x; stA[4 * q + 1] = va.y; stA[4 * q + 2] = va.z; stA[4 * q + 3] = va.w;
+      stB[4 * q] = vb.x; stB[4 * q + 1] = vb.y; stB[4 * q + 2] = vb.z; stB[4 * q + 3] = vb.w;
+    }
+  }
+
+  float sqA = 0.0f, sqB = 0.0f;
 #pragma unroll 4
   for (int i = 0; i < 32; ++i) {
-    float acc = s_pb[i];
-#pragma unroll
-    for (int kp = 0; kp < 8; ++kp) acc = fdot2(s_proj[kp * 32 + i], z2[kp], acc);
-    f16x2 sv = __builtin_bit_cast(f16x2, stv[i >> 1]);
-    float d = (float)sv[i & 1] - acc;
-    sqsum += d * d;
-  }
-
-  float hd[16];
-#pragma unroll
-  for (int i = 0; i < 16; ++i) hd[i] = 0.0f;
+    const uint4* pw = (const uint4*)&s_proj[i * 8];
+    uint4 w0 = pw[0], w1 = pw[1];
+    float aA = s_pb[i], aB = s_pb[i];
+    DOT4(aA, w0.x, w0.y, w0.z, w0.w, *(const uint4*)&zA[0]);
+    DOT4(aA, w1.x, w1.y, w1.z, w1.w, *(const uint4*)&zA[4]);
+    DOT4(aB, w0.x, w0.y, w0.z, w0.w, *(const uint4*)&zB[0]);
+    DOT4(aB, w1.x, w1.y, w1.z, w1.w, *(const uint4*)&zB[4]);
+    f16x2 svA = __builtin_bit_cast(f16x2, stA[i >> 1]);
+    f16x2 svB = __builtin_bit_cast(f16x2, stB[i >> 1]);
+    float dA = (float)svA[i & 1] - aA;
+    float dB = (float)svB[i & 1] - aB;
+    sqA += dA * dA;
+    sqB += dB * dB;
+  }
+
+  float hdA[16], hdB[16];
+#pragma unroll
+  for (int i = 0; i < 16; ++i) { hdA[i] = 0.0f; hdB[i] = 0.0f; }
 #pragma unroll 2
   for (int j = 0; j < 128; ++j) {
-    float a = s_ab[j];
-#pragma unroll
-    for (int kp = 0; kp < 8; ++kp) a = fdot2(s_act[kp * 128 + j], z2[kp], a);
-    a = fmaxf(a, 0.0f);
+    const uint4* aw = (const uint4*)&s_act[j * 8];
+    uint4 w0 = aw[0], w1 = aw[1];
+    float aA = s_ab[j], aB = s_ab[j];
+    DOT4(aA, w0.x, w0.y, w0.z, w0.w, *(const uint4*)&zA[0]);
+    DOT4(aA, w1.x, w1.y, w1.z, w1.w, *(const uint4*)&zA[4]);
+    DOT4(aB, w0.x, w0.y, w0.z, w0.w, *(const uint4*)&zB[0]);
+    DOT4(aB, w1.x, w1.y, w1.z, w1.w, *(const uint4*)&zB[4]);
+    aA = fmaxf(aA, 0.0f);
+    aB = fmaxf(aB, 0.0f);
+    const uint4* hw = (const uint4*)&s_head[j * 8];
+    uint4 h0 = hw[0], h1 = hw[1];
+    uint32_t whu[8] = {h0.x, h0.y, h0.z, h0.w, h1.x, h1.y, h1.z, h1.w};
 #pragma unroll
     for (int p = 0; p < 8; ++p) {
-      f16x2 w = __builtin_bit_cast(f16x2, s_head[j * 8 + p]);
-      hd[2 * p] += (float)w[0] * a;
-      hd[2 * p + 1] += (float)w[1] * a;
-    }
-  }
-  const float* xp = xs + idx * 23;
-  float dl0 = hd[0] - xp[18], dl1 = hd[1] - xp[19];
-  float land = dl0 * dl0 + dl1 * dl1;
-  float dm0 = hd[14] - xp[21], dm1 = hd[15] - xp[22];
-  float move = dm0 * dm0 + dm1 * dm1;
-  int sid = (int)xp[20];
-  float m = hd[2];
-#pragma unroll
-  for (int s = 1; s < 12; ++s) m = fmaxf(m, hd[2 + s]);
-  float sume = 0.0f;
-#pragma unroll
-  for (int s = 0; s < 12; ++s) sume += __expf(hd[2 + s] - m);
-  float lse = m + __logf(sume);
-  float pl = 0.0f;
-#pragma unroll
-  for (int s = 0; s < 12; ++s)
-    if (s == sid) pl = hd[2 + s];
-  float picked = 0.0f, cnt = 0.0f;
-  if (sid != 0) {
-    picked = pl - lse;
-    cnt = 1.0f;
-  }
-  float vals[5] = {sqsum, land, move, picked, cnt};
+      f16x2 w = __builtin_bit_cast(f16x2, whu[p]);
+      float w0f = (float)w[0], w1f = (float)w[1];
+      hdA[2 * p] += w0f * aA;
+      hdA[2 * p + 1] += w1f * aA;
+      hdB[2 * p] += w0f * aB;
+      hdB[2 * p + 1] += w1f * aB;
+    }
+  }
+
+  float vals[5] = {sqA + sqB, 0.f, 0.f, 0.f, 0.f};
+#pragma unroll
+  for (int tok = 0; tok < 2; ++tok) {
+    const float* hd = tok ? hdB : hdA;
+    const float* xp = xs + (tok ? idx1 : idx0) * 23;
+    float dl0 = hd[0] - xp[18], dl1 = hd[1] - xp[19];
+    vals[1] += dl0 * dl0 + dl1 * dl1;
+    float dm0 = hd[14] - xp[21], dm1 = hd[15] - xp[22];
+    vals[2] += dm0 * dm0 + dm1 * dm1;
+    int sid = (int)xp[20];
+    float m = hd[2];
+#pragma unroll
+    for (int s = 1; s < 12; ++s) m = fmaxf(m, hd[2 + s]);
+    float sume = 0.0f;
+#pragma unroll
+    for (int s = 0; s < 12; ++s) sume += __expf(hd[2 + s] - m);
+    float lse = m + __logf(sume);
+    float pl = 0.0f;
+#pragma unroll
+    for (int s = 0; s < 12; ++s)
+      if (s == sid) pl = hd[2 + s];
+    if (sid != 0) {
+      vals[3] += pl - lse;
+      vals[4] += 1.0f;
+    }
+  }
 #pragma unroll
   for (int v = 0; v < 5; ++v) {
     float x = vals[v];
@@ -657,13 +598,13 @@
   f16* zs = (f16*)(ws + 256 + 16777216 + 33554432 + 32768);
 
   k_embed<<<1024, 256, 0, stream>>>(xs, shot_emb, player_emb, state_t, accums);
-  k_gru<<<256, 512, 0, stream>>>(state_t, gru_wih, gru_whh, gru_bih, gru_bhh,
+  k_gru<<<512, 448, 0, stream>>>(state_t, gru_wih, gru_whh, gru_bih, gru_bhh,
                                  enc_w, enc_b, qz0_w, qz0_b, z0_noise, pz0_mean,
                                  pz0_logstd, ctx, z0b, accums);
-  k_sde<<<256, 512, 0, stream>>>(ctx, z0b, ts, bm_noise, f_w1, f_b1, f_w2, f_b2,
+  k_sde<<<512, 256, 0, stream>>>(ctx, z0b, ts, bm_noise, f_w1, f_b1, f_w2, f_b2,
                                  f_w3, f_b3, h_w1, h_b1, h_w2, h_b2, h_w3, h_b3,
                                  g_w1, g_b1, g_w2, g_b2, zs, accums);
-  k_dec<<<1024, 256, 0, stream>>>(zs, state_t, xs, proj_w, proj_b, act_w, act_b,
-                                  act_land_w, act_shot_w, act_move_w, accums);
+  k_dec<<<512, 256, 0, stream>>>(zs, state_t, xs, proj_w, proj_b, act_w, act_b,
+                                 act_land_w, act_shot_w, act_move_w, accums);
   k_fin<<<1, 64, 0, stream>>>(accums, noise_std, (float*)d_out);
 }
```

Measured after the change: 2.005 ms. Within noise of the previous version (+0.3%).
